# Performance work log

Hardware: AMD Instinct MI355X
Metric: run time of the kernel (lower is better)

Reference implementation:

```python
import jax, jax.numpy as jnp
import numpy as np

NUM_ROUTING = 3
EPS = 1e-8


def squash(s, axis):
    # s * (||s||^2 / (1 + ||s||^2)) / ||s||  along `axis`
    sq = jnp.sum(s * s, axis=axis, keepdims=True)
    return s * (sq / (1.0 + sq)) / jnp.sqrt(sq + EPS)


def setup_inputs() -> dict:
    key = jax.random.key(0)
    k1, k2 = jax.random.split(key)
    B, R, C, OUT, IN = 32, 2048, 32, 32, 16
    x = jax.random.normal(k1, (B, R, IN), dtype=jnp.float32)
    vote = jax.random.normal(k2, (R, C, OUT, IN), dtype=jnp.float32)
    return {"x": x, "vote": vote}


def reference(x, vote):
    # votes[b,r,c,o] = sum_i vote[r,c,o,i] * x[b,r,i]
    votes = jnp.einsum('rcoi,bri->brco', vote, x)  # [B,R,C,OUT]
    agreement = jnp.zeros_like(votes)
    verdict = None
    for _ in range(NUM_ROUTING):
        chairman = jax.nn.softmax(agreement, axis=1)          # softmax over routes
        summary = jnp.sum(chairman * votes, axis=1, keepdims=True)  # [B,1,C,OUT]
        verdict = squash(summary, axis=3)                     # squash over out_dim
        agreement = agreement + jnp.sum(votes * verdict, axis=3, keepdims=True)
    return verdict[:, 0, :, :]  # [B, C, OUT]
```

## Files before the change

### kernel.cpp

```cpp
#include <hip/hip_runtime.h>
#include <hip/hip_fp16.h>

#define B 32
#define R 2048
#define C 32
#define O 32
#define IN 16

typedef _Float16 hf2 __attribute__((ext_vector_type(2)));


__global__ __launch_bounds__(512, 4) void votes_kernel(
    const float* __restrict__ x,
    const float* __restrict__ vote,
    __half* __restrict__ votes_h)
{
  const int t = threadIdx.x;
  const int c = blockIdx.y * 2 + (t >> 8);
  const int tt = t & 255;
  const int rp_l = tt >> 4;
  const int op = tt & 15;
  const int r0 = blockIdx.x * 32;
  const int r = r0 + 2 * rp_l;
  const int rpg = blockIdx.x * 16 + rp_l;

  __shared__ unsigned int x_lds[32 * 32 * 8];

#pragma unroll
  for (int k = 0; k < 8; ++k) {
    int j = t + k * 512;
    int bb = j >> 7;
    int rr = (j >> 2) & 31;
    int ic = j & 3;
    float4 v = *reinterpret_cast<const float4*>(
        x + ((size_t)bb * R + r0 + rr) * IN + ic * 4);
    __half2 h01 = __float22half2_rn(make_float2(v.x, v.y));
    __half2 h23 = __float22half2_rn(make_float2(v.z, v.w));
    int w = (bb * 32 + rr) * 8 + 2 * ic;
    x_lds[w] = __builtin_bit_cast(unsigned int, h01);
    x_lds[w + 1] = __builtin_bit_cast(unsigned int, h23);
  }

  unsigned int wh[4][8];
#pragma unroll
  for (int p = 0; p < 2; ++p) {
#pragma unroll
    for (int q = 0; q < 2; ++q) {
      const float4* vp = reinterpret_cast<const float4*>(
          vote + (((size_t)(r + p) * C + c) * O + 2 * op + q) * IN);
#pragma unroll
      for (int k = 0; k < 4; ++k) {
        float4 f = vp[k];
        __half2 a = __float22half2_rn(make_float2(f.x, f.y));
        __half2 d = __float22half2_rn(make_float2(f.z, f.w));
        wh[p * 2 + q][2 * k] = __builtin_bit_cast(unsigned int, a);
        wh[p * 2 + q][2 * k + 1] = __builtin_bit_cast(unsigned int, d);
      }
    }
  }
  __syncthreads();

  __half* ob = votes_h + (size_t)c * 65536 + (size_t)rpg * 64 + op * 4;

#pragma unroll 2
  for (int bb = 0; bb < 32; ++bb) {
    const uint4* xr = reinterpret_cast<const uint4*>(
        &x_lds[(bb * 32 + 2 * rp_l) * 8]);
    uint4 xa = xr[0], xb = xr[1];
    uint4 xc = xr[2], xd = xr[3];
    unsigned int x0[8] = {xa.x, xa.y, xa.z, xa.w, xb.x, xb.y, xb.z, xb.w};
    unsigned int x1[8] = {xc.x, xc.y, xc.z, xc.w, xd.x, xd.y, xd.z, xd.w};
    float a00 = 0.f, a01 = 0.f, a10 = 0.f, a11 = 0.f;
#pragma unroll
    for (int k = 0; k < 8; ++k) {
      hf2 xv0 = __builtin_bit_cast(hf2, x0[k]);
      hf2 xv1 = __builtin_bit_cast(hf2, x1[k]);
      a00 = __builtin_amdgcn_fdot2(__builtin_bit_cast(hf2, wh[0][k]), xv0, a00, false);
      a01 = __builtin_amdgcn_fdot2(__builtin_bit_cast(hf2, wh[1][k]), xv0, a01, false);
      a10 = __builtin_amdgcn_fdot2(__builtin_bit_cast(hf2, wh[2][k]), xv1, a10, false);
      a11 = __builtin_amdgcn_fdot2(__builtin_bit_cast(hf2, wh[3][k]), xv1, a11, false);
    }
    __half2 w0 = __float22half2_rn(make_float2(a00, a10));
    __half2 w1 = __float22half2_rn(make_float2(a01, a11));
    uint2 pk;
    pk.x = __builtin_bit_cast(unsigned int, w0);
    pk.y = __builtin_bit_cast(unsigned int, w1);
    *reinterpret_cast<uint2*>(ob + (size_t)bb * C * 65536) = pk;
  }
}

__global__ __launch_bounds__(1024, 4) void routing_kernel(
    const __half* __restrict__ votes_h,
    float* __restrict__ out)
{
  const int b = blockIdx.x >> 5;
  const int c = blockIdx.x & 31;
  const int t = threadIdx.x;
  const int lane = t & 63;
  const int wave = t >> 6;
  const int g = t >> 5;
  const int o = t & 31;

  __shared__ unsigned int vmix[1024 * 34];
  __shared__ float2 e2[1024];
  __shared__ float red[32][33];
  __shared__ float vdf[32];
  __shared__ float scal_z[16];

  const uint4* src = reinterpret_cast<const uint4*>(
      votes_h + ((size_t)b * C + c) * 65536);
#pragma unroll
  for (int k = 0; k < 8; ++k) {
    int j = t + k * 1024;
    uint4 v = src[j];
    int rp = j >> 3;
    int q = j & 7;
    unsigned int* dst = &vmix[rp * 34 + 4 * q];
    uint2 a; a.x = v.x; a.y = v.y;
    uint2 d; d.x = v.z; d.y = v.w;
    *reinterpret_cast<uint2*>(dst) = a;
    *reinterpret_cast<uint2*>(dst + 2) = d;
  }
  __syncthreads();

  float a0 = 0.0f, a1 = 0.0f;
  float Zinv = 1.0f / 2048.0f;

  for (int iter = 0; iter < 3; ++iter) {
    if (iter > 0) {
      float e0 = __expf(a0), e1 = __expf(a1);
      float z = e0 + e1;
#pragma unroll
      for (int mask = 32; mask; mask >>= 1) z += __shfl_xor(z, mask);
      if (lane == 0) scal_z[wave] = z;
      e2[t] = make_float2(e0, e1);
      __syncthreads();
      float Z = 0.0f;
#pragma unroll
      for (int w = 0; w < 16; ++w) Z += scal_z[w];
      Zinv = 1.0f / Z;
    }

    {
      float s = 0.0f;
      const unsigned int* vb = &vmix[(size_t)g * 32 * 34 + o];
      if (iter == 0) {
#pragma unroll
        for (int j = 0; j < 32; ++j) {
          __half2 vv = __builtin_bit_cast(__half2, vb[j * 34]);
          s += __low2float(vv) + __high2float(vv);
        }
      } else {
        const float2* eb = &e2[g * 32];
#pragma unroll
        for (int j = 0; j < 32; ++j) {
          __half2 vv = __builtin_bit_cast(__half2, vb[j * 34]);
          float2 ee = eb[j];
          s += ee.x * __low2float(vv) + ee.y * __high2float(vv);
        }
      }
      red[o][g] = s;
    }
    __syncthreads();

    if (t < 32) {
      float S = 0.0f;
#pragma unroll
      for (int gg = 0; gg < 32; ++gg) S += red[t][gg];
      float summary = S * Zinv;
      float sq = summary * summary;
#pragma unroll
      for (int mask = 16; mask; mask >>= 1) sq += __shfl_xor(sq, mask);
      float scale = sq / ((1.0f + sq) * sqrtf(sq + 1e-8f));
      float vd = summary * scale;
      vdf[t] = vd;
      if (iter == 2) out[((size_t)b * C + c) * O + t] = vd;
    }
    __syncthreads();

    if (iter < 2) {
      float u0 = 0.0f, u1 = 0.0f;
      const unsigned int* vb = &vmix[(size_t)t * 34];
#pragma unroll
      for (int q = 0; q < 16; ++q) {
        uint2 vv = *reinterpret_cast<const uint2*>(vb + 2 * q);
        __half2 va = __builtin_bit_cast(__half2, vv.x);
        __half2 vbh = __builtin_bit_cast(__half2, vv.y);
        float vda = vdf[2 * q], vdb = vdf[2 * q + 1];
        u0 += __low2float(va) * vda + __low2float(vbh) * vdb;
        u1 += __high2float(va) * vda + __high2float(vbh) * vdb;
      }
      a0 += u0;
      a1 += u1;
    }
  }
}

extern "C" void kernel_launch(void* const* d_in, const int* in_sizes, int n_in,
                              void* d_out, int out_size, void* d_ws, size_t ws_size,
                              hipStream_t stream) {
  const float* x = (const float*)d_in[0];
  const float* vote = (const float*)d_in[1];
  float* out = (float*)d_out;
  __half* votes_h = (__half*)d_ws;

  votes_kernel<<<dim3(R / 32, C / 2), 512, 0, stream>>>(x, vote, votes_h);
  routing_kernel<<<dim3(B * C), 1024, 0, stream>>>(votes_h, out);
}
```

Before: 281.8 us.

## Keep routing votes in registers with shuffle reductions and shrink votes-kernel blocks

The routing kernel no longer stages each (b,c) vote slab in a large padded LDS array. Each thread keeps 8 uint4 of votes in registers, and the reductions over routes and output dims use wave shuffles plus a butterfly scatter-reduce, which frees LDS for higher occupancy. The votes kernel is halved to 256-thread blocks over 16 routes with a smaller x tile. The trade is higher register pressure in the routing kernel, more shuffle instructions, and the ordering of the vdf write against its read now relies on the sync placed inside the iter<2 branch.

```diff
diff --git a/kernel.cpp b/kernel.cpp
--- a/kernel.cpp
+++ b/kernel.cpp
@@ -10,33 +10,33 @@
 typedef _Float16 hf2 __attribute__((ext_vector_type(2)));
 
 
-__global__ __launch_bounds__(512, 4) void votes_kernel(
+__global__ __launch_bounds__(256, 8) void votes_kernel(
     const float* __restrict__ x,
     const float* __restrict__ vote,
     __half* __restrict__ votes_h)
 {
   const int t = threadIdx.x;
-  const int c = blockIdx.y * 2 + (t >> 8);
-  const int tt = t & 255;
+  const int c = blockIdx.y * 2 + (t >> 7);
+  const int tt = t & 127;
   const int rp_l = tt >> 4;
-  const int op = tt & 15;
-  const int r0 = blockIdx.x * 32;
+  const int op = t & 15;
+  const int r0 = blockIdx.x * 16;
   const int r = r0 + 2 * rp_l;
-  const int rpg = blockIdx.x * 16 + rp_l;
-
-  __shared__ unsigned int x_lds[32 * 32 * 8];
+  const int rpg = blockIdx.x * 8 + rp_l;
+
+  __shared__ unsigned int x_lds[32 * 16 * 8];
 
 #pragma unroll
   for (int k = 0; k < 8; ++k) {
-    int j = t + k * 512;
-    int bb = j >> 7;
-    int rr = (j >> 2) & 31;
+    int j = t + k * 256;
+    int bb = j >> 6;
+    int rr = (j >> 2) & 15;
     int ic = j & 3;
     float4 v = *reinterpret_cast<const float4*>(
         x + ((size_t)bb * R + r0 + rr) * IN + ic * 4);
     __half2 h01 = __float22half2_rn(make_float2(v.x, v.y));
     __half2 h23 = __float22half2_rn(make_float2(v.z, v.w));
-    int w = (bb * 32 + rr) * 8 + 2 * ic;
+    int w = (bb * 16 + rr) * 8 + 2 * ic;
     x_lds[w] = __builtin_bit_cast(unsigned int, h01);
     x_lds[w + 1] = __builtin_bit_cast(unsigned int, h23);
   }
@@ -45,16 +45,16 @@
 #pragma unroll
   for (int p = 0; p < 2; ++p) {
 #pragma unroll
-    for (int q = 0; q < 2; ++q) {
+    for (int qq = 0; qq < 2; ++qq) {
       const float4* vp = reinterpret_cast<const float4*>(
-          vote + (((size_t)(r + p) * C + c) * O + 2 * op + q) * IN);
+          vote + (((size_t)(r + p) * C + c) * O + 2 * op + qq) * IN);
 #pragma unroll
       for (int k = 0; k < 4; ++k) {
         float4 f = vp[k];
         __half2 a = __float22half2_rn(make_float2(f.x, f.y));
         __half2 d = __float22half2_rn(make_float2(f.z, f.w));
-        wh[p * 2 + q][2 * k] = __builtin_bit_cast(unsigned int, a);
-        wh[p * 2 + q][2 * k + 1] = __builtin_bit_cast(unsigned int, d);
+        wh[p * 2 + qq][2 * k] = __builtin_bit_cast(unsigned int, a);
+        wh[p * 2 + qq][2 * k + 1] = __builtin_bit_cast(unsigned int, d);
       }
     }
   }
@@ -65,7 +65,7 @@
 #pragma unroll 2
   for (int bb = 0; bb < 32; ++bb) {
     const uint4* xr = reinterpret_cast<const uint4*>(
-        &x_lds[(bb * 32 + 2 * rp_l) * 8]);
+        &x_lds[(bb * 16 + 2 * rp_l) * 8]);
     uint4 xa = xr[0], xb = xr[1];
     uint4 xc = xr[2], xd = xr[3];
     unsigned int x0[8] = {xa.x, xa.y, xa.z, xa.w, xb.x, xb.y, xb.z, xb.w};
@@ -89,7 +89,28 @@
   }
 }
 
-__global__ __launch_bounds__(1024, 4) void routing_kernel(
+__device__ __forceinline__ float rscatter8(const float u[8], int q) {
+  const bool h4 = (q & 4) != 0;
+  const bool h2 = (q & 2) != 0;
+  const bool h1 = (q & 1) != 0;
+  float ka = h4 ? u[4] : u[0], sa = h4 ? u[0] : u[4];
+  float kb = h4 ? u[5] : u[1], sb = h4 ? u[1] : u[5];
+  float kc = h4 ? u[6] : u[2], sc = h4 ? u[2] : u[6];
+  float kd = h4 ? u[7] : u[3], sd = h4 ? u[3] : u[7];
+  ka += __shfl_xor(sa, 4);
+  kb += __shfl_xor(sb, 4);
+  kc += __shfl_xor(sc, 4);
+  kd += __shfl_xor(sd, 4);
+  float pa = h2 ? kc : ka, qa = h2 ? ka : kc;
+  float pb = h2 ? kd : kb, qb = h2 ? kb : kd;
+  pa += __shfl_xor(qa, 2);
+  pb += __shfl_xor(qb, 2);
+  float ra = h1 ? pb : pa, rs = h1 ? pa : pb;
+  ra += __shfl_xor(rs, 1);
+  return ra;
+}
+
+__global__ __launch_bounds__(1024, 8) void routing_kernel(
     const __half* __restrict__ votes_h,
     float* __restrict__ out)
 {
@@ -98,34 +119,23 @@
   const int t = threadIdx.x;
   const int lane = t & 63;
   const int wave = t >> 6;
-  const int g = t >> 5;
-  const int o = t & 31;
-
-  __shared__ unsigned int vmix[1024 * 34];
-  __shared__ float2 e2[1024];
-  __shared__ float red[32][33];
+  const int q = t & 7;
+  const int rb = t >> 3;
+
+  __shared__ float2 e2s[1024];
+  __shared__ float4 red4[16][8];
   __shared__ float vdf[32];
   __shared__ float scal_z[16];
 
   const uint4* src = reinterpret_cast<const uint4*>(
       votes_h + ((size_t)b * C + c) * 65536);
-#pragma unroll
-  for (int k = 0; k < 8; ++k) {
-    int j = t + k * 1024;
-    uint4 v = src[j];
-    int rp = j >> 3;
-    int q = j & 7;
-    unsigned int* dst = &vmix[rp * 34 + 4 * q];
-    uint2 a; a.x = v.x; a.y = v.y;
-    uint2 d; d.x = v.z; d.y = v.w;
-    *reinterpret_cast<uint2*>(dst) = a;
-    *reinterpret_cast<uint2*>(dst + 2) = d;
-  }
-  __syncthreads();
-
-  float a0 = 0.0f, a1 = 0.0f;
-  float Zinv = 1.0f / 2048.0f;
-
+  uint4 v[8];
+#pragma unroll
+  for (int k = 0; k < 8; ++k) v[k] = src[rb * 64 + k * 8 + q];
+
+  float a0 = 0.f, a1 = 0.f;
+
+#pragma unroll
   for (int iter = 0; iter < 3; ++iter) {
     if (iter > 0) {
       float e0 = __expf(a0), e1 = __expf(a1);
@@ -133,65 +143,94 @@
 #pragma unroll
       for (int mask = 32; mask; mask >>= 1) z += __shfl_xor(z, mask);
       if (lane == 0) scal_z[wave] = z;
-      e2[t] = make_float2(e0, e1);
+      e2s[rb * 8 + q] = make_float2(e0, e1);
       __syncthreads();
-      float Z = 0.0f;
-#pragma unroll
-      for (int w = 0; w < 16; ++w) Z += scal_z[w];
-      Zinv = 1.0f / Z;
-    }
-
-    {
-      float s = 0.0f;
-      const unsigned int* vb = &vmix[(size_t)g * 32 * 34 + o];
+    }
+
+    float s0 = 0.f, s1 = 0.f, s2 = 0.f, s3 = 0.f;
+    if (iter == 0) {
+#pragma unroll
+      for (int k = 0; k < 8; ++k) {
+        __half2 h0 = __builtin_bit_cast(__half2, v[k].x);
+        __half2 h1 = __builtin_bit_cast(__half2, v[k].y);
+        __half2 h2 = __builtin_bit_cast(__half2, v[k].z);
+        __half2 h3 = __builtin_bit_cast(__half2, v[k].w);
+        s0 += __low2float(h0) + __high2float(h0);
+        s1 += __low2float(h1) + __high2float(h1);
+        s2 += __low2float(h2) + __high2float(h2);
+        s3 += __low2float(h3) + __high2float(h3);
+      }
+    } else {
+#pragma unroll
+      for (int k = 0; k < 8; ++k) {
+        float2 e = e2s[rb * 8 + k];
+        __half2 h0 = __builtin_bit_cast(__half2, v[k].x);
+        __half2 h1 = __builtin_bit_cast(__half2, v[k].y);
+        __half2 h2 = __builtin_bit_cast(__half2, v[k].z);
+        __half2 h3 = __builtin_bit_cast(__half2, v[k].w);
+        s0 += e.x * __low2float(h0) + e.y * __high2float(h0);
+        s1 += e.x * __low2float(h1) + e.y * __high2float(h1);
+        s2 += e.x * __low2float(h2) + e.y * __high2float(h2);
+        s3 += e.x * __low2float(h3) + e.y * __high2float(h3);
+      }
+    }
+    s0 += __shfl_xor(s0, 8);  s1 += __shfl_xor(s1, 8);
+    s2 += __shfl_xor(s2, 8);  s3 += __shfl_xor(s3, 8);
+    s0 += __shfl_xor(s0, 16); s1 += __shfl_xor(s1, 16);
+    s2 += __shfl_xor(s2, 16); s3 += __shfl_xor(s3, 16);
+    s0 += __shfl_xor(s0, 32); s1 += __shfl_xor(s1, 32);
+    s2 += __shfl_xor(s2, 32); s3 += __shfl_xor(s3, 32);
+    if (lane < 8) red4[wave][lane] = make_float4(s0, s1, s2, s3);
+    __syncthreads();
+
+    if (t < 32) {
+      const float* redf = reinterpret_cast<const float*>(red4);
+      float S = 0.f;
+#pragma unroll
+      for (int w = 0; w < 16; ++w) S += redf[w * 32 + t];
+      float Zinv;
       if (iter == 0) {
-#pragma unroll
-        for (int j = 0; j < 32; ++j) {
-          __half2 vv = __builtin_bit_cast(__half2, vb[j * 34]);
-          s += __low2float(vv) + __high2float(vv);
-        }
+        Zinv = 1.0f / 2048.0f;
       } else {
-        const float2* eb = &e2[g * 32];
-#pragma unroll
-        for (int j = 0; j < 32; ++j) {
-          __half2 vv = __builtin_bit_cast(__half2, vb[j * 34]);
-          float2 ee = eb[j];
-          s += ee.x * __low2float(vv) + ee.y * __high2float(vv);
-        }
-      }
-      red[o][g] = s;
-    }
-    __syncthreads();
-
-    if (t < 32) {
-      float S = 0.0f;
-#pragma unroll
-      for (int gg = 0; gg < 32; ++gg) S += red[t][gg];
+        float Z = 0.f;
+#pragma unroll
+        for (int w = 0; w < 16; ++w) Z += scal_z[w];
+        Zinv = 1.0f / Z;
+      }
       float summary = S * Zinv;
       float sq = summary * summary;
 #pragma unroll
       for (int mask = 16; mask; mask >>= 1) sq += __shfl_xor(sq, mask);
       float scale = sq / ((1.0f + sq) * sqrtf(sq + 1e-8f));
       float vd = summary * scale;
-      vdf[t] = vd;
-      if (iter == 2) out[((size_t)b * C + c) * O + t] = vd;
-    }
-    __syncthreads();
+      if (iter < 2) vdf[t] = vd;
+      else out[((size_t)b * C + c) * O + t] = vd;
+    }
 
     if (iter < 2) {
-      float u0 = 0.0f, u1 = 0.0f;
-      const unsigned int* vb = &vmix[(size_t)t * 34];
-#pragma unroll
-      for (int q = 0; q < 16; ++q) {
-        uint2 vv = *reinterpret_cast<const uint2*>(vb + 2 * q);
-        __half2 va = __builtin_bit_cast(__half2, vv.x);
-        __half2 vbh = __builtin_bit_cast(__half2, vv.y);
-        float vda = vdf[2 * q], vdb = vdf[2 * q + 1];
-        u0 += __low2float(va) * vda + __low2float(vbh) * vdb;
-        u1 += __high2float(va) * vda + __high2float(vbh) * vdb;
-      }
-      a0 += u0;
-      a1 += u1;
+      __syncthreads();
+      float4 vd4 = *reinterpret_cast<const float4*>(&vdf[4 * q]);
+      float u[8];
+#pragma unroll
+      for (int k = 0; k < 8; ++k) {
+        __half2 h0 = __builtin_bit_cast(__half2, v[k].x);
+        __half2 h1 = __builtin_bit_cast(__half2, v[k].y);
+        __half2 h2 = __builtin_bit_cast(__half2, v[k].z);
+        __half2 h3 = __builtin_bit_cast(__half2, v[k].w);
+        u[k] = __low2float(h0) * vd4.x + __low2float(h1) * vd4.y +
+               __low2float(h2) * vd4.z + __low2float(h3) * vd4.w;
+      }
+      a0 += rscatter8(u, q);
+#pragma unroll
+      for (int k = 0; k < 8; ++k) {
+        __half2 h0 = __builtin_bit_cast(__half2, v[k].x);
+        __half2 h1 = __builtin_bit_cast(__half2, v[k].y);
+        __half2 h2 = __builtin_bit_cast(__half2, v[k].z);
+        __half2 h3 = __builtin_bit_cast(__half2, v[k].w);
+        u[k] = __high2float(h0) * vd4.x + __high2float(h1) * vd4.y +
+               __high2float(h2) * vd4.z + __high2float(h3) * vd4.w;
+      }
+      a1 += rscatter8(u, q);
     }
   }
 }
@@ -204,6 +243,6 @@
   float* out = (float*)d_out;
   __half* votes_h = (__half*)d_ws;
 
-  votes_kernel<<<dim3(R / 32, C / 2), 512, 0, stream>>>(x, vote, votes_h);
+  votes_kernel<<<dim3(R / 16, C / 2), 256, 0, stream>>>(x, vote, votes_h);
   routing_kernel<<<dim3(B * C), 1024, 0, stream>>>(votes_h, out);
 }
```

After: 409.5 us. +45.3%, slower.
